# Kernel optimization log

Measured on AMD Instinct MI355X. Metric: run time of the kernel, lower is better.

## Reference

```python
import jax, jax.numpy as jnp
import numpy as np
import math

M = 0.4      # angular margin
S = 64.0     # scale
K = 0.7      # virtual-prototype damping
START_VP_EPOCH = 4


def _l2norm(v, eps):
    # F.normalize: v / max(||v||_2, eps), row-wise
    n = jnp.sqrt(jnp.sum(v * v, axis=-1, keepdims=True))
    return v / jnp.maximum(n, eps)


def setup_inputs() -> dict:
    key = jax.random.key(0)
    k1, k2, k3, k4 = jax.random.split(key, 4)
    B, D, C = 256, 512, 100000
    return {
        "x": jax.random.normal(k1, (B, D), dtype=jnp.float32),
        "labels": jax.random.randint(k2, (B,), 0, C),
        "weight": jax.random.normal(k3, (C, D), dtype=jnp.float32) * 0.05,
        "queue": jax.random.normal(k4, (C, D), dtype=jnp.float32),
        "epoch": 5,
    }


def reference(x, labels, weight, queue, epoch):
    labels = labels.astype(jnp.int32)
    C = weight.shape[0]

    emb = _l2norm(x, 1e-5)                                   # [B, D]
    cosine = emb @ _l2norm(weight, 1e-5).T                   # [B, C]
    cosine = jnp.clip(cosine, -1.0 + 1e-7, 1.0 - 1e-7)

    # --- update_virtual_prototype (fully detached in the original) ---
    emb_d = jax.lax.stop_gradient(emb)
    q_rows = queue[labels]                                   # [B, D] gather
    # diag(queue[labels] @ emb.T) == rowwise dot (avoid O(B^2) matmul)
    drift = jnp.sum(q_rows * emb_d, axis=1)                  # [B]
    factor = (drift / (1.0 + jnp.abs(drift)))[:, None]       # softsign
    new_rows = _l2norm(factor * q_rows + (1.0 - factor) * emb_d, 1e-12)
    queue = queue.at[labels].set(new_rows)

    if epoch + 1 >= START_VP_EPOCH:
        qn = jax.lax.stop_gradient(_l2norm(queue, 1e-12))    # [C, D]
        vp_sim = emb @ qn.T                                  # [B, C]
        B = vp_sim.shape[0]
        rows = jnp.arange(B)
        diag = vp_sim[rows, labels]
        # v - k * v.detach()  ->  value (1-k)*v, grad passes as identity
        vp_sim = vp_sim.at[rows, labels].set(diag - K * jax.lax.stop_gradient(diag))
        cosine = jnp.concatenate([cosine, vp_sim], axis=0)   # [2B, C]
        labels = jnp.concatenate([labels, labels], axis=0)

    one_hot = labels[:, None] == jnp.arange(C)[None, :]      # [N, C] bool

    sine = jnp.sqrt(jnp.clip(1.0 - cosine * cosine, 0.0, 1.0))
    cosine_m = cosine * math.cos(M) - sine * math.sin(M)
    # characteristic_gradient_detachment: value = cosine_m, grad = d(cosine)
    phi = cosine - jax.lax.stop_gradient(cosine) + jax.lax.stop_gradient(cosine_m)

    logits = jnp.where(one_hot, phi, cosine) * S             # [N, C]

    # EPL loss with one-hot targets
    oh = one_hot.astype(logits.dtype)
    sum_neg = jnp.sum((1.0 - oh) * jnp.exp(logits), axis=1)  # [N]
    sum_pos = jnp.sum(oh * jnp.exp(-logits), axis=1)         # [N]
    loss = jnp.log(1.0 + sum_neg * sum_pos)
    return jnp.mean(loss)
```

## Files before the change

kernel.cpp:

```cpp
#include <hip/hip_runtime.h>
#include <hip/hip_bf16.h>

#define D_DIM 512
#define NROWS 256
#define NT 32
#define KSTEPS 16
#define S_SCALE 64.0f
#define COS_M 0.9210609940028851f
#define SIN_M 0.3894183423086505f

typedef short short8 __attribute__((ext_vector_type(8)));
typedef float f32x4 __attribute__((ext_vector_type(4)));

typedef const __attribute__((address_space(1))) void* gas1_t;
typedef __attribute__((address_space(3))) void* las3_t;

static __device__ __forceinline__ void gload16(const void* g, void* l){
  __builtin_amdgcn_global_load_lds((gas1_t)g, (las3_t)l, 16, 0, 0);
}

static __device__ __forceinline__ short f2bf(float f){
  __hip_bfloat16 h = __float2bfloat16(f);
  return __builtin_bit_cast(short, h);
}

__global__ void k_emb(const float* __restrict__ x, float* __restrict__ emb,
                      short* __restrict__ embA){
  int b = blockIdx.x, t = threadIdx.x;
  float v0 = x[b*D_DIM + t];
  float v1 = x[b*D_DIM + 256 + t];
  __shared__ float red[256];
  red[t] = v0*v0 + v1*v1;
  __syncthreads();
  for (int o=128;o>0;o>>=1){ if(t<o) red[t]+=red[t+o]; __syncthreads(); }
  float inv = 1.0f / fmaxf(sqrtf(red[0]), 1e-5f);
  float e0 = v0*inv, e1 = v1*inv;
  emb[b*D_DIM + t]       = e0;
  emb[b*D_DIM + 256 + t] = e1;
  int rb = b >> 4;
  {
    int d=t; int ks=d>>5, kg=(d>>3)&3, j=d&7;
    int lane=(kg<<4)|(b&15);
    embA[((ks*16+rb)*64+lane)*8+j] = f2bf(e0);
  }
  {
    int d=t+256; int ks=d>>5, kg=(d>>3)&3, j=d&7;
    int lane=(kg<<4)|(b&15);
    embA[((ks*16+rb)*64+lane)*8+j] = f2bf(e1);
  }
}

__global__ void k_init(int* __restrict__ upd, int C){
  int i = blockIdx.x*256 + threadIdx.x;
  if (i < C) upd[i] = -1;
}

__global__ void k_vp(const float* __restrict__ queue, const float* __restrict__ emb,
                     const int* __restrict__ labels, float* __restrict__ newrow,
                     int* __restrict__ upd){
  int b = blockIdx.x, t = threadIdx.x;
  int lab = labels[b];
  const float* q = queue + (size_t)lab * D_DIM;
  float q0=q[t], q1=q[t+256];
  float e0=emb[b*D_DIM+t], e1=emb[b*D_DIM+256+t];
  __shared__ float red[256];
  __shared__ int win;
  red[t] = q0*e0 + q1*e1;
  __syncthreads();
  for (int o=128;o>0;o>>=1){ if(t<o) red[t]+=red[t+o]; __syncthreads(); }
  float drift = red[0];
  float fac = drift / (1.0f + fabsf(drift));
  float v0 = fac*q0 + (1.0f-fac)*e0;
  float v1 = fac*q1 + (1.0f-fac)*e1;
  __syncthreads();
  if (t==0) win = 1;
  red[t] = v0*v0 + v1*v1;
  __syncthreads();
  for (int o=128;o>0;o>>=1){ if(t<o) red[t]+=red[t+o]; __syncthreads(); }
  float inv = 1.0f / fmaxf(sqrtf(red[0]), 1e-12f);
  newrow[b*D_DIM+t]     = v0*inv;
  newrow[b*D_DIM+256+t] = v1*inv;
  if (t > b && labels[t] == lab) win = 0;
  __syncthreads();
  if (t==0 && win) upd[lab] = b;
}

__global__ __launch_bounds__(256,3) void k_main(
    const float* __restrict__ W, const float* __restrict__ Q,
    const short* __restrict__ embA, const float* __restrict__ newrow,
    const int* __restrict__ upd, const int* __restrict__ labels,
    float* __restrict__ partials, float* __restrict__ posval,
    int C, int nwg)
{
  __shared__ __align__(16) char ldsb[2*8192];
  const int wg   = blockIdx.x;
  const int tid  = threadIdx.x;
  const int wave = tid >> 6;
  const int lane = tid & 63;
  const int lcol = lane & 15;
  const int lkg  = lane >> 4;
  const int c0 = wg * NT;
  const int m0 = wave * 64;

  const char* ssrc[2];
  int sdst[2];
#pragma unroll
  for (int i=0;i<2;i++){
    int ch  = wave*2 + i;
    int mat = ch >> 2;
    int r   = (ch&3)*8 + (lane>>3);
    int gs  = (lane&7) ^ (lane>>3);
    int cls = c0 + r; if (cls >= C) cls = C-1;
    const float* rowp;
    if (mat == 0) rowp = W + (size_t)cls * D_DIM;
    else {
      int u = upd[cls];
      rowp = (u >= 0) ? (newrow + (size_t)u * D_DIM) : (Q + (size_t)cls * D_DIM);
    }
    ssrc[i] = (const char*)(rowp + gs*4);
    sdst[i] = ch * 1024;
  }

  const short8* Af = reinterpret_cast<const short8*>(embA);
  const f32x4 vzero = {0.f,0.f,0.f,0.f};
  f32x4 accW[4][2], accQ[4][2];
#pragma unroll
  for (int i=0;i<4;i++)
#pragma unroll
    for (int j=0;j<2;j++){ accW[i][j]=vzero; accQ[i][j]=vzero; }
  float wss[2] = {0.f,0.f};
  float qss[2] = {0.f,0.f};

  short8 afc[4], afn[4];
#pragma unroll
  for (int i=0;i<2;i++) gload16(ssrc[i], ldsb + sdst[i]);
#pragma unroll
  for (int rb=0;rb<4;rb++) afc[rb] = Af[(wave*4 + rb)*64 + lane];
  __syncthreads();

  for (int ks=0; ks<KSTEPS; ++ks){
    const int cur = ks & 1;
    if (ks+1 < KSTEPS){
#pragma unroll
      for (int i=0;i<2;i++)
        gload16(ssrc[i] + (ks+1)*128, ldsb + (cur^1)*8192 + sdst[i]);
#pragma unroll
      for (int rb=0;rb<4;rb++) afn[rb] = Af[((ks+1)*16 + wave*4 + rb)*64 + lane];
    }
    const char* bb = ldsb + cur*8192;
#pragma unroll
    for (int cb=0;cb<2;cb++){
      const int row = cb*16 + lcol;
      const int s   = row & 7;
      const int g0  = lkg*2;
      const f32x4 w0 = *(const f32x4*)(bb + row*128 + (((g0  )^s)*16));
      const f32x4 w1 = *(const f32x4*)(bb + row*128 + (((g0+1)^s)*16));
      const f32x4 z0 = *(const f32x4*)(bb + 4096 + row*128 + (((g0  )^s)*16));
      const f32x4 z1 = *(const f32x4*)(bb + 4096 + row*128 + (((g0+1)^s)*16));
      wss[cb] += w0[0]*w0[0]+w0[1]*w0[1]+w0[2]*w0[2]+w0[3]*w0[3]
               + w1[0]*w1[0]+w1[1]*w1[1]+w1[2]*w1[2]+w1[3]*w1[3];
      qss[cb] += z0[0]*z0[0]+z0[1]*z0[1]+z0[2]*z0[2]+z0[3]*z0[3]
               + z1[0]*z1[0]+z1[1]*z1[1]+z1[2]*z1[2]+z1[3]*z1[3];
      short8 bw, bq;
#pragma unroll
      for (int j=0;j<4;j++){
        bw[j] = f2bf(w0[j]); bw[j+4] = f2bf(w1[j]);
        bq[j] = f2bf(z0[j]); bq[j+4] = f2bf(z1[j]);
      }
#pragma unroll
      for (int rb=0;rb<4;rb++)
        accW[rb][cb] = __builtin_amdgcn_mfma_f32_16x16x32_bf16(afc[rb], bw, accW[rb][cb], 0, 0, 0);
#pragma unroll
      for (int rb=0;rb<4;rb++)
        accQ[rb][cb] = __builtin_amdgcn_mfma_f32_16x16x32_bf16(afc[rb], bq, accQ[rb][cb], 0, 0, 0);
    }
    __syncthreads();
#pragma unroll
    for (int rb=0;rb<4;rb++) afc[rb] = afn[rb];
  }

  float winv[2], qinv[2];
#pragma unroll
  for (int cb=0;cb<2;cb++){
    float w = wss[cb]; w += __shfl_xor(w, 16); w += __shfl_xor(w, 32);
    float q = qss[cb]; q += __shfl_xor(q, 16); q += __shfl_xor(q, 32);
    winv[cb] = 1.0f / fmaxf(sqrtf(w), 1e-5f);
    qinv[cb] = 1.0f / fmaxf(sqrtf(q), 1e-12f);
  }

#pragma unroll
  for (int rb=0;rb<4;rb++){
#pragma unroll
    for (int r=0;r<4;r++){
      const int m = m0 + rb*16 + lkg*4 + r;
      const int lab = labels[m];
      float nw = 0.f, nq = 0.f;
#pragma unroll
      for (int cb=0;cb<2;cb++){
        int c = c0 + cb*16 + lcol;
        if (c < C){
          float cw = accW[rb][cb][r] * winv[cb];
          cw = fminf(fmaxf(cw, -1.0f + 1e-7f), 1.0f - 1e-7f);
          float cq = accQ[rb][cb][r] * qinv[cb];
          if (c == lab){
            float sw  = sqrtf(fminf(fmaxf(1.0f - cw*cw, 0.0f), 1.0f));
            float phw = cw*COS_M - sw*SIN_M;
            posval[m] = __expf(-S_SCALE*phw);
            float vq  = 0.3f * cq;
            float sq  = sqrtf(fminf(fmaxf(1.0f - vq*vq, 0.0f), 1.0f));
            float phq = vq*COS_M - sq*SIN_M;
            posval[NROWS + m] = __expf(-S_SCALE*phq);
          } else {
            nw += __expf(S_SCALE*cw);
            nq += __expf(S_SCALE*cq);
          }
        }
      }
#pragma unroll
      for (int msk=1; msk<16; msk<<=1){
        nw += __shfl_xor(nw, msk);
        nq += __shfl_xor(nq, msk);
      }
      if (lcol == 0){
        partials[(size_t)wg*512 + m]       = nw;
        partials[(size_t)wg*512 + 256 + m] = nq;
      }
    }
  }
}

__global__ void k_red(const float* __restrict__ partials, const float* __restrict__ posval,
                      float* __restrict__ lossv, int nwg){
  int n = blockIdx.x, t = threadIdx.x;
  float s = 0.f;
  for (int i=t; i<nwg; i+=256) s += partials[(size_t)i*512 + n];
  __shared__ float red[256];
  red[t] = s; __syncthreads();
  for (int o=128;o>0;o>>=1){ if(t<o) red[t]+=red[t+o]; __syncthreads(); }
  if (t==0) lossv[n] = logf(1.0f + red[0] * posval[n]);
}

__global__ void k_fin(const float* __restrict__ lossv, const int* __restrict__ epoch,
                      float* __restrict__ out){
  int t = threadIdx.x;
  int N = (epoch[0] + 1 >= 4) ? 2*NROWS : NROWS;
  float v = (t < N) ? lossv[t] : 0.f;
  __shared__ float red[512];
  red[t] = v; __syncthreads();
  for (int o=256;o>0;o>>=1){ if(t<o) red[t]+=red[t+o]; __syncthreads(); }
  if (t==0) out[0] = red[0] / (float)N;
}

extern "C" void kernel_launch(void* const* d_in, const int* in_sizes, int n_in,
                              void* d_out, int out_size, void* d_ws, size_t ws_size,
                              hipStream_t stream)
{
  const float* x      = (const float*)d_in[0];
  const int*   labels = (const int*)d_in[1];
  const float* W      = (const float*)d_in[2];
  const float* Q      = (const float*)d_in[3];
  const int*   epoch  = (const int*)d_in[4];
  float* out = (float*)d_out;
  const int C   = in_sizes[2] / D_DIM;
  const int nwg = (C + NT - 1) / NT;

  char* ws = (char*)d_ws;
  float* emb      = (float*)(ws + 0);
  short* embA     = (short*)(ws + 524288);
  float* newrow   = (float*)(ws + 786432);
  int*   upd      = (int*)  (ws + 1310720);
  float* posval   = (float*)(ws + 1712128);
  float* lossv    = (float*)(ws + 1714176);
  float* partials = (float*)(ws + 1716224);

  hipLaunchKernelGGL(k_emb,  dim3(NROWS),       dim3(256), 0, stream, x, emb, embA);
  hipLaunchKernelGGL(k_init, dim3((C+255)/256), dim3(256), 0, stream, upd, C);
  hipLaunchKernelGGL(k_vp,   dim3(NROWS),       dim3(256), 0, stream, Q, emb, labels, newrow, upd);
  hipLaunchKernelGGL(k_main, dim3(nwg),         dim3(256), 0, stream,
                     W, Q, embA, newrow, upd, labels, partials, posval, C, nwg);
  hipLaunchKernelGGL(k_red,  dim3(2*NROWS),     dim3(256), 0, stream, partials, posval, lossv, nwg);
  hipLaunchKernelGGL(k_fin,  dim3(1),           dim3(512), 0, stream, lossv, epoch, out);
}
```

Before: 176.4 us.

## Deepen LDS pipeline to four stages and compute row norms via MFMA

Switches the staging buffer from a double buffer to a 4-slot ring with three tiles in flight. The per-step __syncthreads is replaced by explicit vmcnt waits plus a single barrier, and sched_barriers pin the instruction order. The scalar FMA sum-of-squares for the weight and queue row norms is replaced by an extra bf16 MFMA of each B fragment with itself, with the diagonal then extracted by a shuffle. This aims to hide global-load latency and cut VALU work. It doubles LDS use, which may lower occupancy, and the norms are now computed from bf16-rounded values.

```diff
diff --git a/kernel.cpp b/kernel.cpp
--- a/kernel.cpp
+++ b/kernel.cpp
@@ -92,7 +92,7 @@
     float* __restrict__ partials, float* __restrict__ posval,
     int C, int nwg)
 {
-  __shared__ __align__(16) char ldsb[2*8192];
+  __shared__ __align__(16) char ldsb[4*8192];
   const int wg   = blockIdx.x;
   const int tid  = threadIdx.x;
   const int wave = tid >> 6;
@@ -120,34 +120,49 @@
     ssrc[i] = (const char*)(rowp + gs*4);
     sdst[i] = ch * 1024;
   }
+  __builtin_amdgcn_sched_barrier(0);
 
   const short8* Af = reinterpret_cast<const short8*>(embA);
   const f32x4 vzero = {0.f,0.f,0.f,0.f};
-  f32x4 accW[4][2], accQ[4][2];
+  f32x4 accW[4][2], accQ[4][2], accNW[2], accNQ[2];
 #pragma unroll
   for (int i=0;i<4;i++)
 #pragma unroll
     for (int j=0;j<2;j++){ accW[i][j]=vzero; accQ[i][j]=vzero; }
-  float wss[2] = {0.f,0.f};
-  float qss[2] = {0.f,0.f};
+  accNW[0]=vzero; accNW[1]=vzero; accNQ[0]=vzero; accNQ[1]=vzero;
 
   short8 afc[4], afn[4];
 #pragma unroll
-  for (int i=0;i<2;i++) gload16(ssrc[i], ldsb + sdst[i]);
-#pragma unroll
   for (int rb=0;rb<4;rb++) afc[rb] = Af[(wave*4 + rb)*64 + lane];
-  __syncthreads();
-
+  __builtin_amdgcn_sched_barrier(0);
+#pragma unroll
+  for (int t=0;t<3;t++){
+#pragma unroll
+    for (int i=0;i<2;i++)
+      gload16(ssrc[i] + t*128, ldsb + t*8192 + sdst[i]);
+    __builtin_amdgcn_sched_barrier(0);
+  }
+
+#pragma unroll
   for (int ks=0; ks<KSTEPS; ++ks){
-    const int cur = ks & 1;
+    if (ks == 0)            asm volatile("s_waitcnt vmcnt(4)" ::: "memory");
+    else if (ks < KSTEPS-2) asm volatile("s_waitcnt vmcnt(2)" ::: "memory");
+    else                    asm volatile("s_waitcnt vmcnt(0)" ::: "memory");
+    __builtin_amdgcn_s_barrier();
+    __builtin_amdgcn_sched_barrier(0);
     if (ks+1 < KSTEPS){
 #pragma unroll
+      for (int rb=0;rb<4;rb++) afn[rb] = Af[((ks+1)*16 + wave*4 + rb)*64 + lane];
+    }
+    __builtin_amdgcn_sched_barrier(0);
+    if (ks+3 < KSTEPS){
+#pragma unroll
       for (int i=0;i<2;i++)
-        gload16(ssrc[i] + (ks+1)*128, ldsb + (cur^1)*8192 + sdst[i]);
-#pragma unroll
-      for (int rb=0;rb<4;rb++) afn[rb] = Af[((ks+1)*16 + wave*4 + rb)*64 + lane];
-    }
-    const char* bb = ldsb + cur*8192;
+        gload16(ssrc[i] + (ks+3)*128, ldsb + ((ks+3)&3)*8192 + sdst[i]);
+    }
+    __builtin_amdgcn_sched_barrier(0);
+
+    const char* bb = ldsb + (ks&3)*8192;
 #pragma unroll
     for (int cb=0;cb<2;cb++){
       const int row = cb*16 + lcol;
@@ -157,16 +172,14 @@
       const f32x4 w1 = *(const f32x4*)(bb + row*128 + (((g0+1)^s)*16));
       const f32x4 z0 = *(const f32x4*)(bb + 4096 + row*128 + (((g0  )^s)*16));
       const f32x4 z1 = *(const f32x4*)(bb + 4096 + row*128 + (((g0+1)^s)*16));
-      wss[cb] += w0[0]*w0[0]+w0[1]*w0[1]+w0[2]*w0[2]+w0[3]*w0[3]
-               + w1[0]*w1[0]+w1[1]*w1[1]+w1[2]*w1[2]+w1[3]*w1[3];
-      qss[cb] += z0[0]*z0[0]+z0[1]*z0[1]+z0[2]*z0[2]+z0[3]*z0[3]
-               + z1[0]*z1[0]+z1[1]*z1[1]+z1[2]*z1[2]+z1[3]*z1[3];
       short8 bw, bq;
 #pragma unroll
       for (int j=0;j<4;j++){
         bw[j] = f2bf(w0[j]); bw[j+4] = f2bf(w1[j]);
         bq[j] = f2bf(z0[j]); bq[j+4] = f2bf(z1[j]);
       }
+      accNW[cb] = __builtin_amdgcn_mfma_f32_16x16x32_bf16(bw, bw, accNW[cb], 0, 0, 0);
+      accNQ[cb] = __builtin_amdgcn_mfma_f32_16x16x32_bf16(bq, bq, accNQ[cb], 0, 0, 0);
 #pragma unroll
       for (int rb=0;rb<4;rb++)
         accW[rb][cb] = __builtin_amdgcn_mfma_f32_16x16x32_bf16(afc[rb], bw, accW[rb][cb], 0, 0, 0);
@@ -174,7 +187,6 @@
       for (int rb=0;rb<4;rb++)
         accQ[rb][cb] = __builtin_amdgcn_mfma_f32_16x16x32_bf16(afc[rb], bq, accQ[rb][cb], 0, 0, 0);
     }
-    __syncthreads();
 #pragma unroll
     for (int rb=0;rb<4;rb++) afc[rb] = afn[rb];
   }
@@ -182,10 +194,14 @@
   float winv[2], qinv[2];
 #pragma unroll
   for (int cb=0;cb<2;cb++){
-    float w = wss[cb]; w += __shfl_xor(w, 16); w += __shfl_xor(w, 32);
-    float q = qss[cb]; q += __shfl_xor(q, 16); q += __shfl_xor(q, 32);
-    winv[cb] = 1.0f / fmaxf(sqrtf(w), 1e-5f);
-    qinv[cb] = 1.0f / fmaxf(sqrtf(q), 1e-12f);
+    int rsel = lcol & 3;
+    float vw = rsel==0?accNW[cb][0]:rsel==1?accNW[cb][1]:rsel==2?accNW[cb][2]:accNW[cb][3];
+    float vq = rsel==0?accNQ[cb][0]:rsel==1?accNQ[cb][1]:rsel==2?accNQ[cb][2]:accNQ[cb][3];
+    int src = ((lcol>>2)<<4) | lcol;
+    float ssW = __shfl(vw, src);
+    float ssQ = __shfl(vq, src);
+    winv[cb] = 1.0f / fmaxf(sqrtf(ssW), 1e-5f);
+    qinv[cb] = 1.0f / fmaxf(sqrtf(ssQ), 1e-12f);
   }
 
 #pragma unroll
```

After: 165.8 us. 1.06x faster.
